# Kernel optimization log

Measured on AMD Instinct MI355X. Metric: run time of the kernel, lower is better.

Reference implementation:

```python
import jax, jax.numpy as jnp
import numpy as np

L, H, E, FF, MAXP, NKNOW = 4, 8, 512, 2048, 10, 1000
B, S = 4, 128
HD = E // H


def _layer_norm(x, g, b, eps=1e-5):
    m = x.mean(-1, keepdims=True)
    v = ((x - m) ** 2).mean(-1, keepdims=True)
    return (x - m) / jnp.sqrt(v + eps) * g + b


def setup_inputs() -> dict:
    key = jax.random.key(0)
    ks = jax.random.split(key, 16)
    x = jax.random.normal(ks[0], (B, S, E), jnp.float32)
    adj = jax.random.randint(ks[1], (B, S, S), 0, 2, jnp.int32)
    s_mask = jax.random.randint(ks[2], (B, S, S), 0, 2, jnp.int32)
    o_mask = jax.random.randint(ks[3], (B, S, S), 0, 2, jnp.int32)
    knowledge = jax.random.normal(ks[4], (NKNOW, E), jnp.float32)
    know_adj = jax.random.randint(ks[5], (B, S, S), 0, NKNOW, jnp.int64)
    pos_mask = jax.random.randint(ks[6], (S, S), 0, MAXP + 1, jnp.int32)
    # relative position embedding tables (padding_idx=0 -> row 0 zero)
    pe_k = jax.random.normal(ks[7], (MAXP + 1, HD), jnp.float32).at[0].set(0.0)
    pe_v = jax.random.normal(ks[8], (MAXP + 1, HD), jnp.float32).at[0].set(0.0)
    sc = 0.02
    # stacked per-layer parameters
    Wq = jax.random.normal(ks[9], (L, E, E), jnp.float32) * sc
    Wk = jax.random.normal(ks[10], (L, E, E), jnp.float32) * sc
    Wvs = jax.random.normal(ks[11], (L, E, E), jnp.float32) * sc
    Wvo = jax.random.normal(ks[12], (L, E, E), jnp.float32) * sc
    Wo = jax.random.normal(ks[13], (L, E, E), jnp.float32) * sc
    Wkn = jax.random.normal(ks[14], (L, E, E), jnp.float32) * sc
    kf = jax.random.split(ks[15], 4)
    w1 = jax.random.normal(kf[0], (L, FF, E), jnp.float32) * sc
    b1 = jnp.zeros((L, FF), jnp.float32)
    w2 = jax.random.normal(kf[1], (L, E, FF), jnp.float32) * sc
    b2 = jnp.zeros((L, E), jnp.float32)
    ln1_g = jnp.ones((L, E), jnp.float32)
    ln1_b = jnp.zeros((L, E), jnp.float32)
    ln2_g = jnp.ones((L, E), jnp.float32)
    ln2_b = jnp.zeros((L, E), jnp.float32)
    return dict(x=x, adj=adj, s_mask=s_mask, o_mask=o_mask, knowledge=knowledge,
                know_adj=know_adj, pos_mask=pos_mask, pe_k=pe_k, pe_v=pe_v,
                Wq=Wq, Wk=Wk, Wvs=Wvs, Wvo=Wvo, Wo=Wo, Wkn=Wkn,
                ln1_g=ln1_g, ln1_b=ln1_b, w1=w1, b1=b1, w2=w2, b2=b2,
                ln2_g=ln2_g, ln2_b=ln2_b)


def reference(x, adj, s_mask, o_mask, knowledge, know_adj, pos_mask, pe_k, pe_v,
              Wq, Wk, Wvs, Wvo, Wo, Wkn, ln1_g, ln1_b, w1, b1, w2, b2,
              ln2_g, ln2_b):
    bsz, slen, emb = x.shape
    hd = emb // H
    scaling = float(hd) ** (-0.5)
    # relative position embeddings, shared across batch/heads: [S,S,hd]
    pos = jnp.clip(pos_mask, 0, MAXP)
    rel_k = pe_k[pos]
    rel_v = pe_v[pos]
    adj_f = adj.astype(x.dtype)[:, None, :, :]          # [B,1,S,S]
    sm = s_mask.astype(x.dtype)[:, None, :, :, None]    # [B,1,S,S,1]
    om = o_mask.astype(x.dtype)[:, None, :, :, None]
    know_feat = knowledge[know_adj]                      # [B,S,S,E]

    def split_heads(t):  # [B,S,E] -> [B,H,S,hd]
        return t.reshape(bsz, slen, H, hd).transpose(0, 2, 1, 3)

    h = x
    for i in range(L):
        q = split_heads(h @ Wq[i].T)
        k = split_heads(h @ Wk[i].T)
        vs = split_heads(h @ Wvs[i].T)
        vo = split_heads(h @ Wvo[i].T)
        # knowledge projection -> [B,H,S,S,hd]
        know = (know_feat @ Wkn[i].T).reshape(bsz, slen, slen, H, hd).transpose(0, 3, 1, 2, 4)
        # multiplicative attention: q_i * (k_j + know_ij + rel_ij) summed over hd
        rel = (know + rel_k[None, None]) + k[:, :, None, :, :]
        scores = jnp.einsum('bhid,bhijd->bhij', q, rel) * scaling
        scores = scores - (1.0 - adj_f) * 1e30          # mask_logic
        attn = jax.nn.softmax(scores, axis=-1)           # [B,H,S,S]
        value = vs[:, :, None, :, :] * sm + vo[:, :, None, :, :] * om  # [B,H,S,S,hd]
        attn_sum = jnp.einsum('bhijd,bhij->bhid', value + rel_v[None, None], attn)
        out = attn_sum.transpose(0, 2, 1, 3).reshape(bsz, slen, emb) @ Wo[i].T
        h = _layer_norm(h + out, ln1_g[i], ln1_b[i])
        ff = jax.nn.relu(h @ w1[i].T + b1[i]) @ w2[i].T + b2[i]
        h = _layer_norm(h + ff, ln2_g[i], ln2_b[i])
    return h
```

## Files before the change

kernel.cpp:

```cpp
#include <hip/hip_runtime.h>

#define EE 512
#define SS 128
#define BB 4
#define NH 8
#define HD 64
#define FFD 2048
#define NL 4
#define LDQ 2048

typedef short bf16x8 __attribute__((ext_vector_type(8)));
typedef float f32x4 __attribute__((ext_vector_type(4)));

__device__ __forceinline__ ushort f2bf(float f) {
    uint u = __float_as_uint(f);
    return (ushort)((u + 0x7fffu + ((u >> 16) & 1u)) >> 16);
}
__device__ __forceinline__ float bflo(uint u) { return __uint_as_float(u << 16); }
__device__ __forceinline__ float bfhi(uint u) { return __uint_as_float(u & 0xffff0000u); }

__device__ __forceinline__ void gll16(const ushort* g, ushort* l) {
    __builtin_amdgcn_global_load_lds(
        (const __attribute__((address_space(1))) void*)g,
        (__attribute__((address_space(3))) void*)l, 16, 0, 0);
}

struct GemmJob {
    const ushort* A; const ushort* B;
    float* Cf; ushort* Cb;
    const float* bias; const float* resid;
    int M, N, K, flags, nbx, base;
};

__global__ __launch_bounds__(256) void gemm_bf16(GemmJob j0, GemmJob j1, int njobs)
{
    constexpr int BM = 32;
    __shared__ ushort As[2][8 * BM * 8];
    __shared__ ushort Bs[2][8 * 64 * 8];
    GemmJob j = (njobs > 1 && (int)blockIdx.x >= j1.base) ? j1 : j0;
    const int bid = (int)blockIdx.x - j.base;
    const int by = bid / j.nbx, bx = bid % j.nbx;
    const int rowBase = by * BM, colBase = bx * 64;
    const int t = threadIdx.x, lane = t & 63, wid = t >> 6;
    const int wc = wid;
    const int Kd = j.K, Md = j.M, Nd = j.N;

    const ushort* Bg = j.B + (size_t)(colBase + lane) * Kd;
    int gr = rowBase + (lane & 31); if (gr >= Md) gr = Md - 1;
    const ushort* Ag = j.A + (size_t)gr * Kd + (2 * wid + (lane >> 5)) * 8;

    f32x4 acc[2];
#pragma unroll
    for (int m = 0; m < 2; ++m)
#pragma unroll
        for (int r = 0; r < 4; ++r) acc[m][r] = 0.f;

    auto STAGE = [&](int bf, int k0) {
        gll16(Bg + k0 + (2 * wid) * 8,     &Bs[bf][(2 * wid) * 512]);
        gll16(Bg + k0 + (2 * wid + 1) * 8, &Bs[bf][(2 * wid + 1) * 512]);
        gll16(Ag + k0,                     &As[bf][(2 * wid) * 256]);
    };
    auto COMPUTE = [&](int bf) {
#pragma unroll
        for (int kc = 0; kc < 2; ++kc) {
            const int c16 = kc * 4 + (lane >> 4);
            bf16x8 af[2], bfg;
#pragma unroll
            for (int m = 0; m < 2; ++m) {
                const int row = m * 16 + (lane & 15);
                af[m] = *(const bf16x8*)&As[bf][c16 * 256 + row * 8];
            }
            {
                const int rowb = wc * 16 + (lane & 15);
                bfg = *(const bf16x8*)&Bs[bf][c16 * 512 + rowb * 8];
            }
#pragma unroll
            for (int m = 0; m < 2; ++m)
                acc[m] = __builtin_amdgcn_mfma_f32_16x16x32_bf16(af[m], bfg, acc[m], 0, 0, 0);
        }
    };

    const int nt = Kd >> 6;
    STAGE(0, 0);
    __syncthreads();
    int cur = 0;
    for (int tt = 0; tt < nt - 1; ++tt) {
        STAGE(cur ^ 1, (tt + 1) << 6);
        COMPUTE(cur);
        __syncthreads();
        cur ^= 1;
    }
    COMPUTE(cur);

    const int cl = lane & 15, rh = lane >> 4;
#pragma unroll
    for (int m = 0; m < 2; ++m) {
        const int col = colBase + wc * 16 + cl;
        const int row0 = rowBase + m * 16 + rh * 4;
#pragma unroll
        for (int r = 0; r < 4; ++r) {
            const int rr = row0 + r;
            if (rr < Md) {
                float v = acc[m][r];
                if (j.flags & 1) v += j.bias[col];
                if (j.flags & 2) v = fmaxf(v, 0.f);
                if (j.resid) v += j.resid[(size_t)rr * Nd + col];
                if (j.Cf) j.Cf[(size_t)rr * Nd + col] = v;
                if (j.Cb) j.Cb[(size_t)rr * Nd + col] = f2bf(v);
            }
        }
    }
}

struct PrepArgs {
    const float *Wq, *Wk, *Wvs, *Wvo, *Wo, *Wkn, *w1, *w2, *know, *x;
    ushort *wqkvv, *wo, *wkn, *w1b, *w2b, *knowb, *hb;
    float *h;
};
#define P4_WQKVV 1048576
#define P4_B1 (P4_WQKVV + 262144)
#define P4_B2 (P4_B1 + 262144)
#define P4_B3 (P4_B2 + 1048576)
#define P4_B4 (P4_B3 + 1048576)
#define P4_B5 (P4_B4 + 128000)
#define P4_TOT (P4_B5 + 65536)

__global__ __launch_bounds__(256) void prep_kernel(PrepArgs p)
{
    const int i = blockIdx.x * 256 + threadIdx.x;
    if (i >= P4_TOT) return;
    const float4* src;
    ushort4* dst;
    if (i < P4_WQKVV) {
        const int l = i >> 18, r = i & 262143, q = r >> 16;
        const float* s = (q == 0 ? p.Wq : q == 1 ? p.Wk : q == 2 ? p.Wvs : p.Wvo);
        src = (const float4*)s + l * 65536 + (r & 65535);
        dst = (ushort4*)p.wqkvv + i;
    } else if (i < P4_B1) {
        const int k = i - P4_WQKVV;
        src = (const float4*)p.Wo + k; dst = (ushort4*)p.wo + k;
    } else if (i < P4_B2) {
        const int k = i - P4_B1;
        src = (const float4*)p.Wkn + k; dst = (ushort4*)p.wkn + k;
    } else if (i < P4_B3) {
        const int k = i - P4_B2;
        src = (const float4*)p.w1 + k; dst = (ushort4*)p.w1b + k;
    } else if (i < P4_B4) {
        const int k = i - P4_B3;
        src = (const float4*)p.w2 + k; dst = (ushort4*)p.w2b + k;
    } else if (i < P4_B5) {
        const int k = i - P4_B4;
        src = (const float4*)p.know + k; dst = (ushort4*)p.knowb + k;
    } else {
        const int k = i - P4_B5;
        src = (const float4*)p.x + k; dst = (ushort4*)p.hb + k;
        ((float4*)p.h)[k] = *src;
    }
    float4 v = *src;
    ushort4 o; o.x = f2bf(v.x); o.y = f2bf(v.y); o.z = f2bf(v.z); o.w = f2bf(v.w);
    *dst = o;
}

__global__ __launch_bounds__(256) void ln_kernel(
    const float* __restrict__ X, const float* __restrict__ g,
    const float* __restrict__ bt, float* __restrict__ Yf,
    ushort* __restrict__ Yb, int rows)
{
    const int w = threadIdx.x >> 6, lane = threadIdx.x & 63;
    const int row = blockIdx.x * 4 + w;
    if (row >= rows) return;
    const float* x = X + (size_t)row * EE;
    float4 v0 = ((const float4*)x)[lane];
    float4 v1 = ((const float4*)x)[lane + 64];
    float s  = v0.x + v0.y + v0.z + v0.w + v1.x + v1.y + v1.z + v1.w;
    float q2 = v0.x*v0.x + v0.y*v0.y + v0.z*v0.z + v0.w*v0.w
             + v1.x*v1.x + v1.y*v1.y + v1.z*v1.z + v1.w*v1.w;
#pragma unroll
    for (int o = 32; o; o >>= 1) { s += __shfl_xor(s, o); q2 += __shfl_xor(q2, o); }
    const float mean = s * (1.f / EE);
    const float var  = q2 * (1.f / EE) - mean * mean;
    const float rstd = rsqrtf(var + 1e-5f);
    float4 g0 = ((const float4*)g)[lane],  g1 = ((const float4*)g)[lane + 64];
    float4 b0 = ((const float4*)bt)[lane], b1 = ((const float4*)bt)[lane + 64];
    float4 o0, o1;
    o0.x = (v0.x - mean) * rstd * g0.x + b0.x;
    o0.y = (v0.y - mean) * rstd * g0.y + b0.y;
    o0.z = (v0.z - mean) * rstd * g0.z + b0.z;
    o0.w = (v0.w - mean) * rstd * g0.w + b0.w;
    o1.x = (v1.x - mean) * rstd * g1.x + b1.x;
    o1.y = (v1.y - mean) * rstd * g1.y + b1.y;
    o1.z = (v1.z - mean) * rstd * g1.z + b1.z;
    o1.w = (v1.w - mean) * rstd * g1.w + b1.w;
    float* y = Yf + (size_t)row * EE;
    ((float4*)y)[lane] = o0;
    ((float4*)y)[lane + 64] = o1;
    ushort* yb = Yb + (size_t)row * EE;
    ushort4 p0, p1;
    p0.x = f2bf(o0.x); p0.y = f2bf(o0.y); p0.z = f2bf(o0.z); p0.w = f2bf(o0.w);
    p1.x = f2bf(o1.x); p1.y = f2bf(o1.y); p1.z = f2bf(o1.z); p1.w = f2bf(o1.w);
    ((ushort4*)yb)[lane] = p0;
    ((ushort4*)yb)[lane + 64] = p1;
}

__global__ __launch_bounds__(256) void attn_kernel(
    const ushort* __restrict__ qkvv, const ushort* __restrict__ kproj,
    const int* __restrict__ know_adj, const int* __restrict__ pos_mask,
    const float* __restrict__ pe_k, const float* __restrict__ pe_v,
    const int* __restrict__ adj, const int* __restrict__ s_mask,
    const int* __restrict__ o_mask, ushort* __restrict__ asum)
{
    const int blk = blockIdx.x;
    const int b = blk >> 7, i = blk & 127;
    const int t = threadIdx.x;

    __shared__ float q_s[EE];
    __shared__ float sc[NH][SS];
    __shared__ float qpe[NH][11];
    __shared__ float ap[NH][11];
    __shared__ float ws_s[SS], wo_s[SS];
    __shared__ int   pos_s[SS], n_s[SS], adj_s[SS];

    if (t < 64) {
        uint4 v = *(const uint4*)(qkvv + (size_t)(b * SS + i) * LDQ + t * 8);
        float* qd = q_s + t * 8;
        qd[0] = bflo(v.x); qd[1] = bfhi(v.x); qd[2] = bflo(v.y); qd[3] = bfhi(v.y);
        qd[4] = bflo(v.z); qd[5] = bfhi(v.z); qd[6] = bflo(v.w); qd[7] = bfhi(v.w);
    } else if (t >= 128) {
        const int jj = t - 128;
        const size_t off = ((size_t)(b * SS + i)) * SS + jj;
        n_s[jj]   = know_adj[off];
        adj_s[jj] = adj[off];
        ws_s[jj]  = (float)s_mask[off];
        wo_s[jj]  = (float)o_mask[off];
        int p = pos_mask[i * SS + jj];
        pos_s[jj] = p > 10 ? 10 : (p < 0 ? 0 : p);
    }
    __syncthreads();

    if (t < NH * 11) {
        const int h = t / 11, p = t % 11;
        const float* pk = pe_k + p * HD;
        const float* qh = q_s + h * HD;
        float a = 0.f;
#pragma unroll
        for (int d = 0; d < HD; ++d) a += qh[d] * pk[d];
        qpe[h][p] = a;
        ap[h][p] = 0.f;
    }
    __syncthreads();

    {
        const int jj = t >> 1, s = t & 1;
        const uint4* kp4 = (const uint4*)(kproj + (size_t)n_s[jj] * EE + s * 256);
        const uint4* kr4 = (const uint4*)(qkvv + (size_t)(b * SS + jj) * LDQ + EE + s * 256);
        const float amask = adj_s[jj] ? 0.f : 1e30f;
        const int p = pos_s[jj];
#pragma unroll
        for (int h4 = 0; h4 < 4; ++h4) {
            const int h = s * 4 + h4;
            const float* qh = q_s + h * HD;
            float a = 0.f;
#pragma unroll
            for (int dv = 0; dv < 8; ++dv) {
                uint4 kv = kr4[h4 * 8 + dv];
                uint4 pv = kp4[h4 * 8 + dv];
                const float* q8 = qh + dv * 8;
                a += q8[0] * (bflo(kv.x) + bflo(pv.x));
                a += q8[1] * (bfhi(kv.x) + bfhi(pv.x));
                a += q8[2] * (bflo(kv.y) + bflo(pv.y));
                a += q8[3] * (bfhi(kv.y) + bfhi(pv.y));
                a += q8[4] * (bflo(kv.z) + bflo(pv.z));
                a += q8[5] * (bfhi(kv.z) + bfhi(pv.z));
                a += q8[6] * (bflo(kv.w) + bflo(pv.w));
                a += q8[7] * (bfhi(kv.w) + bfhi(pv.w));
            }
            sc[h][jj] = (a + qpe[h][p]) * 0.125f - amask;
        }
    }
    __syncthreads();

    {
        const int w = t >> 6, lane = t & 63;
#pragma unroll
        for (int hh = 0; hh < 2; ++hh) {
            const int h = w * 2 + hh;
            float v0 = sc[h][lane], v1 = sc[h][lane + 64];
            float m = fmaxf(v0, v1);
#pragma unroll
            for (int o = 32; o; o >>= 1) m = fmaxf(m, __shfl_xor(m, o));
            float e0 = __expf(v0 - m), e1 = __expf(v1 - m);
            float ssum = e0 + e1;
#pragma unroll
            for (int o = 32; o; o >>= 1) ssum += __shfl_xor(ssum, o);
            const float inv = 1.f / ssum;
            e0 *= inv; e1 *= inv;
            sc[h][lane] = e0; sc[h][lane + 64] = e1;
            atomicAdd(&ap[h][pos_s[lane]], e0);
            atomicAdd(&ap[h][pos_s[lane + 64]], e1);
        }
    }
    __syncthreads();

    {
        const int h = t >> 5, d0 = (t & 31) * 2;
        float a0 = 0.f, a1 = 0.f;
        const ushort* vbase = qkvv + (size_t)b * SS * LDQ + 1024 + h * HD + d0;
        for (int jj = 0; jj < SS; ++jj) {
            const float aw = sc[h][jj];
            const float wsj = ws_s[jj], woj = wo_s[jj];
            const ushort* r = vbase + (size_t)jj * LDQ;
            const uint vsp = *(const uint*)r;
            const uint vop = *(const uint*)(r + 512);
            a0 += aw * (wsj * bflo(vsp) + woj * bflo(vop));
            a1 += aw * (wsj * bfhi(vsp) + woj * bfhi(vop));
        }
#pragma unroll
        for (int p = 0; p < 11; ++p) {
            const float apv = ap[h][p];
            a0 += apv * pe_v[p * HD + d0];
            a1 += apv * pe_v[p * HD + d0 + 1];
        }
        const uint o = (uint)f2bf(a0) | ((uint)f2bf(a1) << 16);
        *(uint*)(asum + (size_t)(b * SS + i) * EE + h * HD + d0) = o;
    }
}

extern "C" void kernel_launch(void* const* d_in, const int* in_sizes, int n_in,
                              void* d_out, int out_size, void* d_ws, size_t ws_size,
                              hipStream_t stream)
{
    const float* x         = (const float*)d_in[0];
    const int*   adj       = (const int*)d_in[1];
    const int*   s_mask    = (const int*)d_in[2];
    const int*   o_mask    = (const int*)d_in[3];
    const float* knowledge = (const float*)d_in[4];
    const int*   know_adj  = (const int*)d_in[5];
    const int*   pos_mask  = (const int*)d_in[6];
    const float* pe_k      = (const float*)d_in[7];
    const float* pe_v      = (const float*)d_in[8];
    const float* Wq        = (const float*)d_in[9];
    const float* Wk        = (const float*)d_in[10];
    const float* Wvs       = (const float*)d_in[11];
    const float* Wvo       = (const float*)d_in[12];
    const float* Wo        = (const float*)d_in[13];
    const float* Wkn       = (const float*)d_in[14];
    const float* ln1_g     = (const float*)d_in[15];
    const float* ln1_b     = (const float*)d_in[16];
    const float* w1        = (const float*)d_in[17];
    const float* b1        = (const float*)d_in[18];
    const float* w2        = (const float*)d_in[19];
    const float* b2        = (const float*)d_in[20];
    const float* ln2_g     = (const float*)d_in[21];
    const float* ln2_b     = (const float*)d_in[22];

    const int NTOK = BB * SS;
    const size_t NTE = (size_t)NTOK * EE;

    float*  h      = (float*)d_ws;
    float*  xt     = h + NTE;
    ushort* hb     = (ushort*)(xt + NTE);
    ushort* qkvv   = hb + NTE;
    ushort* kprojb = qkvv + (size_t)NTOK * LDQ;
    ushort* asumb  = kprojb + 1024 * EE;
    ushort* ffnb   = asumb + NTE;
    ushort* wqkvv  = ffnb + (size_t)NTOK * FFD;
    ushort* wob    = wqkvv + (size_t)NL * 4 * EE * EE;
    ushort* wknb   = wob + (size_t)NL * EE * EE;
    ushort* w1b    = wknb + (size_t)NL * EE * EE;
    ushort* w2b    = w1b + (size_t)NL * FFD * EE;
    ushort* knowb  = w2b + (size_t)NL * EE * FFD;

    PrepArgs pa;
    pa.Wq = Wq; pa.Wk = Wk; pa.Wvs = Wvs; pa.Wvo = Wvo; pa.Wo = Wo; pa.Wkn = Wkn;
    pa.w1 = w1; pa.w2 = w2; pa.know = knowledge; pa.x = x;
    pa.wqkvv = wqkvv; pa.wo = wob; pa.wkn = wknb; pa.w1b = w1b; pa.w2b = w2b;
    pa.knowb = knowb; pa.hb = hb; pa.h = h;
    prep_kernel<<<dim3((P4_TOT + 255) / 256), dim3(256), 0, stream>>>(pa);

    const dim3 blk(256);
    for (int l = 0; l < NL; ++l) {
        GemmJob jq{};
        jq.A = hb; jq.B = wqkvv + (size_t)l * 4 * EE * EE;
        jq.Cb = qkvv; jq.M = NTOK; jq.N = 4 * EE; jq.K = EE;
        jq.nbx = 32; jq.base = 0;
        GemmJob jk{};
        jk.A = knowb; jk.B = wknb + (size_t)l * EE * EE;
        jk.Cb = kprojb; jk.M = 1000; jk.N = EE; jk.K = EE;
        jk.nbx = 8; jk.base = 512;
        gemm_bf16<<<dim3(768), blk, 0, stream>>>(jq, jk, 2);

        attn_kernel<<<dim3(NTOK), blk, 0, stream>>>(qkvv, kprojb, know_adj, pos_mask,
                                                    pe_k, pe_v, adj, s_mask, o_mask, asumb);

        GemmJob jo{};
        jo.A = asumb; jo.B = wob + (size_t)l * EE * EE;
        jo.Cf = xt; jo.resid = h; jo.M = NTOK; jo.N = EE; jo.K = EE;
        jo.nbx = 8; jo.base = 0;
        gemm_bf16<<<dim3(128), blk, 0, stream>>>(jo, jo, 1);

        ln_kernel<<<dim3(128), blk, 0, stream>>>(xt, ln1_g + l * EE, ln1_b + l * EE,
                                                 h, hb, NTOK);

        GemmJob jf1{};
        jf1.A = hb; jf1.B = w1b + (size_t)l * FFD * EE;
        jf1.Cb = ffnb; jf1.bias = b1 + (size_t)l * FFD; jf1.flags = 3;
        jf1.M = NTOK; jf1.N = FFD; jf1.K = EE; jf1.nbx = 32; jf1.base = 0;
        gemm_bf16<<<dim3(512), blk, 0, stream>>>(jf1, jf1, 1);

        GemmJob jf2{};
        jf2.A = ffnb; jf2.B = w2b + (size_t)l * EE * FFD;
        jf2.Cf = xt; jf2.bias = b2 + (size_t)l * EE; jf2.resid = h; jf2.flags = 1;
        jf2.M = NTOK; jf2.N = EE; jf2.K = FFD; jf2.nbx = 8; jf2.base = 0;
        gemm_bf16<<<dim3(128), blk, 0, stream>>>(jf2, jf2, 1);

        float* lnout = (l == NL - 1) ? (float*)d_out : h;
        ln_kernel<<<dim3(128), blk, 0, stream>>>(xt, ln2_g + l * EE, ln2_b + l * EE,
                                                 lnout, hb, NTOK);
    }
}
```

Before: 554.6 us.

## Batch all-layer knowledge projections upfront and triple-buffer GEMM loads

The knowledge projection for all four layers is now computed once in layer 0 as a single 1000x2048 GEMM fused with the first QKV GEMM. Later layers launch only the QKV GEMM and index their slice with an LDQ stride, removing three separate kproj passes. The GEMM mainloop moves from double to triple buffering with explicit vmcnt waits so loads run two tiles ahead, and the attention value loop is unrolled by 4. The cost is more shared memory per block and a larger kproj workspace buffer.

```diff
diff --git a/kernel.cpp b/kernel.cpp
--- a/kernel.cpp
+++ b/kernel.cpp
@@ -34,13 +34,12 @@
 
 __global__ __launch_bounds__(256) void gemm_bf16(GemmJob j0, GemmJob j1, int njobs)
 {
-    constexpr int BM = 32;
-    __shared__ ushort As[2][8 * BM * 8];
-    __shared__ ushort Bs[2][8 * 64 * 8];
+    __shared__ ushort As[3][2048];
+    __shared__ ushort Bs[3][4096];
     GemmJob j = (njobs > 1 && (int)blockIdx.x >= j1.base) ? j1 : j0;
     const int bid = (int)blockIdx.x - j.base;
     const int by = bid / j.nbx, bx = bid % j.nbx;
-    const int rowBase = by * BM, colBase = bx * 64;
+    const int rowBase = by * 32, colBase = bx * 64;
     const int t = threadIdx.x, lane = t & 63, wid = t >> 6;
     const int wc = wid;
     const int Kd = j.K, Md = j.M, Nd = j.N;
@@ -55,7 +54,8 @@
 #pragma unroll
         for (int r = 0; r < 4; ++r) acc[m][r] = 0.f;
 
-    auto STAGE = [&](int bf, int k0) {
+    auto STAGE = [&](int bf, int tt) {
+        const int k0 = tt << 6;
         gll16(Bg + k0 + (2 * wid) * 8,     &Bs[bf][(2 * wid) * 512]);
         gll16(Bg + k0 + (2 * wid + 1) * 8, &Bs[bf][(2 * wid + 1) * 512]);
         gll16(Ag + k0,                     &As[bf][(2 * wid) * 256]);
@@ -82,15 +82,22 @@
 
     const int nt = Kd >> 6;
     STAGE(0, 0);
-    __syncthreads();
-    int cur = 0;
-    for (int tt = 0; tt < nt - 1; ++tt) {
-        STAGE(cur ^ 1, (tt + 1) << 6);
-        COMPUTE(cur);
-        __syncthreads();
-        cur ^= 1;
-    }
-    COMPUTE(cur);
+    STAGE(1, 1);
+    asm volatile("s_waitcnt vmcnt(3)" ::: "memory");
+    __builtin_amdgcn_s_barrier();
+    int bc = 0, bs = 2;
+    for (int tt = 0; tt < nt; ++tt) {
+        const bool more = (tt + 2) < nt;
+        if (more) STAGE(bs, tt + 2);
+        COMPUTE(bc);
+        if (tt < nt - 1) {
+            if (more) asm volatile("s_waitcnt vmcnt(3)" ::: "memory");
+            else      asm volatile("s_waitcnt vmcnt(0)" ::: "memory");
+            __builtin_amdgcn_s_barrier();
+        }
+        bc = bc == 2 ? 0 : bc + 1;
+        bs = bs == 2 ? 0 : bs + 1;
+    }
 
     const int cl = lane & 15, rh = lane >> 4;
 #pragma unroll
@@ -251,7 +258,7 @@
 
     {
         const int jj = t >> 1, s = t & 1;
-        const uint4* kp4 = (const uint4*)(kproj + (size_t)n_s[jj] * EE + s * 256);
+        const uint4* kp4 = (const uint4*)(kproj + (size_t)n_s[jj] * LDQ + s * 256);
         const uint4* kr4 = (const uint4*)(qkvv + (size_t)(b * SS + jj) * LDQ + EE + s * 256);
         const float amask = adj_s[jj] ? 0.f : 1e30f;
         const int p = pos_s[jj];
@@ -305,6 +312,7 @@
         const int h = t >> 5, d0 = (t & 31) * 2;
         float a0 = 0.f, a1 = 0.f;
         const ushort* vbase = qkvv + (size_t)b * SS * LDQ + 1024 + h * HD + d0;
+#pragma unroll 4
         for (int jj = 0; jj < SS; ++jj) {
             const float aw = sc[h][jj];
             const float wsj = ws_s[jj], woj = wo_s[jj];
@@ -361,7 +369,7 @@
     ushort* hb     = (ushort*)(xt + NTE);
     ushort* qkvv   = hb + NTE;
     ushort* kprojb = qkvv + (size_t)NTOK * LDQ;
-    ushort* asumb  = kprojb + 1024 * EE;
+    ushort* asumb  = kprojb + (size_t)1024 * LDQ;
     ushort* ffnb   = asumb + NTE;
     ushort* wqkvv  = ffnb + (size_t)NTOK * FFD;
     ushort* wob    = wqkvv + (size_t)NL * 4 * EE * EE;
@@ -383,13 +391,18 @@
         jq.A = hb; jq.B = wqkvv + (size_t)l * 4 * EE * EE;
         jq.Cb = qkvv; jq.M = NTOK; jq.N = 4 * EE; jq.K = EE;
         jq.nbx = 32; jq.base = 0;
-        GemmJob jk{};
-        jk.A = knowb; jk.B = wknb + (size_t)l * EE * EE;
-        jk.Cb = kprojb; jk.M = 1000; jk.N = EE; jk.K = EE;
-        jk.nbx = 8; jk.base = 512;
-        gemm_bf16<<<dim3(768), blk, 0, stream>>>(jq, jk, 2);
-
-        attn_kernel<<<dim3(NTOK), blk, 0, stream>>>(qkvv, kprojb, know_adj, pos_mask,
+        if (l == 0) {
+            GemmJob jk{};
+            jk.A = knowb; jk.B = wknb;
+            jk.Cb = kprojb; jk.M = 1000; jk.N = NL * EE; jk.K = EE;
+            jk.nbx = 32; jk.base = 512;
+            gemm_bf16<<<dim3(512 + 1024), blk, 0, stream>>>(jq, jk, 2);
+        } else {
+            gemm_bf16<<<dim3(512), blk, 0, stream>>>(jq, jq, 1);
+        }
+
+        attn_kernel<<<dim3(NTOK), blk, 0, stream>>>(qkvv, kprojb + (size_t)l * EE,
+                                                    know_adj, pos_mask,
                                                     pe_k, pe_v, adj, s_mask, o_mask, asumb);
 
         GemmJob jo{};
```

New measurement: 578.2 us. 4.3% more time.
